# Kernel optimization log

Hardware: AMD Instinct MI355X
Metric: run time of the kernel (lower is better)

## Reference

```python
import jax, jax.numpy as jnp
import numpy as np

N_LAYERS = 2
DEPTH = 4
HIDDEN = 1024
INPUT = 1024
SEQ = 512
BATCH = 64


def setup_inputs() -> dict:
    key = jax.random.key(0)
    k1, k2, k3 = jax.random.split(key, 3)
    x = jax.random.normal(k1, (SEQ, BATCH, INPUT), dtype=jnp.float32)
    state = jnp.zeros((N_LAYERS, BATCH, HIDDEN), dtype=jnp.float32)
    # input_lin (no bias): layer 0 maps INPUT->2H, layers>0 map HIDDEN->2H (equal here)
    w_in = jax.random.normal(k2, (N_LAYERS, INPUT, 2 * HIDDEN), dtype=jnp.float32) * 0.03
    # hidden_lin per depth: HIDDEN->2H with bias
    w_h = jax.random.normal(k3, (N_LAYERS, DEPTH, HIDDEN, 2 * HIDDEN), dtype=jnp.float32) * 0.03
    b_h = jnp.zeros((N_LAYERS, DEPTH, 2 * HIDDEN), dtype=jnp.float32)
    return {"x": x, "state": state, "w_in": w_in, "w_h": w_h, "b_h": b_h}


def _cell(inp, s, w_in_l, w_h_l, b_h_l):
    # inp, s: [B, H]; one RHN cell = DEPTH highway micro-steps
    hg0 = inp @ w_in_l  # [B, 2H], only enters at depth 0
    for d in range(DEPTH):
        hg = s @ w_h_l[d] + b_h_l[d]
        if d == 0:
            hg = hg + hg0
        h = jnp.tanh(hg[:, :HIDDEN])
        g = jax.nn.sigmoid(hg[:, HIDDEN:])
        s = h * g + s * (1.0 - g)  # weight-tied carry: c = 1 - g
    return s


def reference(x, state, w_in, w_h, b_h):
    def step(s_all, x_t):
        inp = x_t
        new_s = []
        for l in range(N_LAYERS):
            s_l = _cell(inp, s_all[l], w_in[l], w_h[l], b_h[l])
            new_s.append(s_l)
            inp = s_l
        new_s = jnp.stack(new_s)  # [n_layers, B, H]
        return new_s, new_s[-1]

    final_s, out = jax.lax.scan(step, state, x)
    return out, final_s
```

## Files before the change

kernel.cpp:

```cpp
#include <hip/hip_runtime.h>
#include <math.h>
#include <stdint.h>


#define SEQ 512
#define NB 64
#define HID 1024
#define NH2 2048
#define NL 2
#define ND 4
#define SBUF (NB * HID)
#define WSLOT ((size_t)NH2 * (size_t)HID)
#define MROWS (SEQ * NB)

typedef _Float16 half8 __attribute__((ext_vector_type(8)));
typedef float float4v __attribute__((ext_vector_type(4)));

#define OFF_HG0 ((size_t)10 * WSLOT * 2)
#define OFF_SSEQ (OFF_HG0 + (size_t)MROWS * NH2 * 2)
#define OFF_MIR (OFF_SSEQ + (size_t)MROWS * HID * 2)
#define OFF_CAR (OFF_MIR + (size_t)4 * SBUF * 2)
#define OFF_CNT (OFF_CAR + (size_t)2 * SBUF * 4)

__device__ __forceinline__ half8 ld8(const _Float16* p) {
    return *reinterpret_cast<const half8*>(p);
}

__device__ __forceinline__ half8 cvt8(const float* p) {
    const float4v a = *reinterpret_cast<const float4v*>(p);
    const float4v b = *reinterpret_cast<const float4v*>(p + 4);
    half8 r;
    r[0] = (_Float16)a[0]; r[1] = (_Float16)a[1];
    r[2] = (_Float16)a[2]; r[3] = (_Float16)a[3];
    r[4] = (_Float16)b[0]; r[5] = (_Float16)b[1];
    r[6] = (_Float16)b[2]; r[7] = (_Float16)b[3];
    return r;
}

__global__ __launch_bounds__(256) void wprep(const float* __restrict__ w_in,
                                             const float* __restrict__ w_h,
                                             _Float16* __restrict__ Wt) {
    const int bid = (int)blockIdx.x;
    const int tk = bid & 31;
    const int tn = (bid >> 5) & 63;
    const int slot = bid >> 11;
    const int l = slot / 5;
    const int j = slot - l * 5;
    const float* __restrict__ src = (j == 0)
        ? (w_in + (size_t)l * WSLOT)
        : (w_h + (size_t)(l * ND + (j - 1)) * WSLOT);
    __shared__ float tile[32][33];
    const int tx = (int)(threadIdx.x & 31u);
    const int ty = (int)(threadIdx.x >> 5);
    const int n = tn * 32 + tx;
#pragma unroll
    for (int r = 0; r < 4; ++r) {
        const int k = tk * 32 + ty + r * 8;
        tile[ty + r * 8][tx] = src[(size_t)k * NH2 + n];
    }
    __syncthreads();
    _Float16* __restrict__ dst = Wt + (size_t)slot * WSLOT;
#pragma unroll
    for (int r = 0; r < 4; ++r) {
        const int nn = tn * 32 + ty + r * 8;
        const int kk = tk * 32 + tx;
        dst[(size_t)nn * HID + kk] = (_Float16)tile[tx][ty + r * 8];
    }
}

__global__ void sinit2(const float* __restrict__ state, _Float16* __restrict__ mir0,
                       float* __restrict__ car0, _Float16* __restrict__ mir1,
                       float* __restrict__ car1, int* __restrict__ cnts) {
    const int i = (int)(blockIdx.x * 256 + threadIdx.x);
    if (i < SBUF) {
        const float v0 = state[i];
        const float v1 = state[SBUF + i];
        mir0[i] = (_Float16)v0; car0[i] = v0;
        mir1[i] = (_Float16)v1; car1[i] = v1;
    }
    if (i < 256) cnts[i] = 0;
}

template <bool AF16>
__global__ __launch_bounds__(256) void gemm_proj(const void* __restrict__ Av,
                                                 const _Float16* __restrict__ Bslot,
                                                 _Float16* __restrict__ C) {
    const int bid = (int)blockIdx.x;
    const int nt = bid & 31;
    const int mt = bid >> 5;
    const int lane = (int)(threadIdx.x & 63u);
    const int wv = (int)(threadIdx.x >> 6);
    const int lr = lane & 15;
    const int kofs = (lane >> 4) * 8;
    const int m = mt * 64 + wv * 16 + lr;
    float4v acc[4];
#pragma unroll
    for (int i = 0; i < 4; ++i) acc[i] = (float4v){0.f, 0.f, 0.f, 0.f};
#pragma unroll 4
    for (int kb = 0; kb < 32; ++kb) {
        half8 a;
        if (AF16) a = ld8((const _Float16*)Av + (size_t)m * HID + kb * 32 + kofs);
        else      a = cvt8((const float*)Av + (size_t)m * HID + kb * 32 + kofs);
#pragma unroll
        for (int ct = 0; ct < 4; ++ct) {
            const int n = nt * 64 + ct * 16 + lr;
            half8 b = ld8(Bslot + (size_t)n * HID + kb * 32 + kofs);
            acc[ct] = __builtin_amdgcn_mfma_f32_16x16x32_f16(a, b, acc[ct], 0, 0, 0);
        }
    }
#pragma unroll
    for (int ct = 0; ct < 4; ++ct) {
#pragma unroll
        for (int i = 0; i < 4; ++i) {
            const int row = mt * 64 + wv * 16 + (lane >> 4) * 4 + i;
            const int col = nt * 64 + ct * 16 + lr;
            const unsigned short mine =
                __builtin_bit_cast(unsigned short, (_Float16)acc[ct][i]);
            const unsigned short oth = (unsigned short)__shfl_xor((int)mine, 1, 64);
            if ((lane & 1) == 0) {
                const uint32_t pk = (uint32_t)mine | ((uint32_t)oth << 16);
                *reinterpret_cast<uint32_t*>(C + (size_t)row * NH2 + col) = pk;
            }
        }
    }
}

__global__ __launch_bounds__(256) void rhn_scan(
    const _Float16* __restrict__ Wt, int slotBase,
    const float* __restrict__ bias,
    const _Float16* __restrict__ hg0,
    _Float16* __restrict__ mirA, _Float16* __restrict__ mirB,
    float* __restrict__ carry,
    int* __restrict__ cnt,
    _Float16* __restrict__ sseq,
    float* __restrict__ outp,
    float* __restrict__ fout) {
    extern __shared__ _Float16 lds[];
    const int wg = (int)blockIdx.x;
    const int d = wg >> 6;
    const int cg = wg & 63;
    const int tid = (int)threadIdx.x;
    const int lane = tid & 63;
    const int m0 = (tid >> 6) * 16;
    const int lr = lane & 15;
    const int kofs = (lane >> 4) * 8;
    const _Float16* __restrict__ slot = Wt + (size_t)(slotBase + d) * WSLOT;

    for (int i = 0; i < 16; ++i) {
        const int flat = i * 256 + tid;
        const int tile = flat >> 11;
        const int kb = (flat >> 6) & 31;
        const int ln = flat & 63;
        const int col = tile * HID + cg * 16 + (ln & 15);
        *reinterpret_cast<half8*>(lds + (size_t)flat * 8) =
            ld8(slot + (size_t)col * HID + kb * 32 + (ln >> 4) * 8);
    }
    __syncthreads();

    const int colh = cg * 16 + lr;
    const float bh = bias[d * NH2 + colh];
    const float bg = bias[d * NH2 + HID + colh];
    const int* __restrict__ pc = cnt + (((d + 3) & 3) * 32);
    int* __restrict__ myc = cnt + d * 32;

    for (int t = 0; t < SEQ; ++t) {
        const int gp = t * 4 + d;

        float pre_h[4], pre_g[4];
        if (d == 0) {
#pragma unroll
            for (int i = 0; i < 4; ++i) {
                const int gr = m0 + (lane >> 4) * 4 + i;
                const size_t hb = (size_t)(t * NB + gr) * NH2 + colh;
                pre_h[i] = (float)hg0[hb];
                pre_g[i] = (float)hg0[hb + HID];
            }
            __asm__ __volatile__("" :: "v"(pre_h[0]), "v"(pre_h[1]), "v"(pre_h[2]),
                                 "v"(pre_h[3]), "v"(pre_g[0]), "v"(pre_g[1]),
                                 "v"(pre_g[2]), "v"(pre_g[3]));
        }

        const int target = (d == 0) ? 64 * t : 64 * (t + 1);
        if (tid == 0) {
            while (__hip_atomic_load(pc, __ATOMIC_RELAXED, __HIP_MEMORY_SCOPE_AGENT) <
                   target) {
            }
        }
        __syncthreads();
        __builtin_amdgcn_fence(__ATOMIC_ACQUIRE, "agent");

        float sold[4];
#pragma unroll
        for (int i = 0; i < 4; ++i) {
            const int gr = m0 + (lane >> 4) * 4 + i;
            sold[i] = __hip_atomic_load(carry + (size_t)gr * HID + colh,
                                        __ATOMIC_RELAXED, __HIP_MEMORY_SCOPE_AGENT);
        }
        __asm__ __volatile__("" :: "v"(sold[0]), "v"(sold[1]), "v"(sold[2]),
                             "v"(sold[3]));

        const _Float16* __restrict__ mr = (gp & 1) ? mirB : mirA;
        const _Float16* __restrict__ arow = mr + (size_t)(m0 + lr) * HID + kofs;
        float4v acch = {0.f, 0.f, 0.f, 0.f};
        float4v accg = {0.f, 0.f, 0.f, 0.f};
#pragma unroll 8
        for (int kb = 0; kb < 32; ++kb) {
            half8 a = ld8(arow + kb * 32);
            half8 bhf = *reinterpret_cast<const half8*>(lds + (size_t)(kb * 64 + lane) * 8);
            half8 bgf =
                *reinterpret_cast<const half8*>(lds + (size_t)((32 + kb) * 64 + lane) * 8);
            acch = __builtin_amdgcn_mfma_f32_16x16x32_f16(a, bhf, acch, 0, 0, 0);
            accg = __builtin_amdgcn_mfma_f32_16x16x32_f16(a, bgf, accg, 0, 0, 0);
        }

        _Float16* __restrict__ mw = ((gp + 1) & 1) ? mirB : mirA;
#pragma unroll
        for (int i = 0; i < 4; ++i) {
            const int gr = m0 + (lane >> 4) * 4 + i;
            const size_t idx = (size_t)gr * HID + colh;
            float ah = acch[i] + bh;
            float ag = accg[i] + bg;
            if (d == 0) {
                ah += pre_h[i];
                ag += pre_g[i];
            }
            const float hv = 1.0f - __fdividef(2.0f, __expf(2.0f * ah) + 1.0f);
            const float gv = __fdividef(1.0f, 1.0f + __expf(-ag));
            const float sn = hv * gv + sold[i] * (1.f - gv);
            __hip_atomic_store(carry + idx, sn, __ATOMIC_RELAXED,
                               __HIP_MEMORY_SCOPE_AGENT);
            const unsigned short mine = __builtin_bit_cast(unsigned short, (_Float16)sn);
            const unsigned short oth = (unsigned short)__shfl_xor((int)mine, 1, 64);
            const uint32_t pk = (uint32_t)mine | ((uint32_t)oth << 16);
            if ((lane & 1) == 0) {
                __hip_atomic_store(reinterpret_cast<uint32_t*>(mw + idx), pk,
                                   __ATOMIC_RELAXED, __HIP_MEMORY_SCOPE_AGENT);
            }
            if (d == 3) {
                if (sseq) {
                    if ((lane & 1) == 0)
                        *reinterpret_cast<uint32_t*>(sseq + (size_t)t * SBUF + idx) = pk;
                } else {
                    outp[(size_t)t * SBUF + idx] = sn;
                }
                if (t == SEQ - 1) fout[idx] = sn;
            }
        }
        __syncthreads();
        if (tid == 0)
            __hip_atomic_fetch_add(myc, 1, __ATOMIC_RELAXED, __HIP_MEMORY_SCOPE_AGENT);
    }
}

extern "C" void kernel_launch(void* const* d_in, const int* in_sizes, int n_in,
                              void* d_out, int out_size, void* d_ws, size_t ws_size,
                              hipStream_t stream) {
    (void)in_sizes; (void)n_in; (void)out_size; (void)ws_size;
    const float* x     = (const float*)d_in[0];
    const float* state = (const float*)d_in[1];
    const float* w_in  = (const float*)d_in[2];
    const float* w_h   = (const float*)d_in[3];
    const float* b_h   = (const float*)d_in[4];
    float* out = (float*)d_out;
    char* ws = (char*)d_ws;
    _Float16* Wt   = (_Float16*)ws;
    _Float16* HG0  = (_Float16*)(ws + OFF_HG0);
    _Float16* Sseq = (_Float16*)(ws + OFF_SSEQ);
    _Float16* mir0a = (_Float16*)(ws + OFF_MIR);
    _Float16* mir0b = mir0a + SBUF;
    _Float16* mir1a = mir0b + SBUF;
    _Float16* mir1b = mir1a + SBUF;
    float* car0 = (float*)(ws + OFF_CAR);
    float* car1 = car0 + SBUF;
    int* cnts = (int*)(ws + OFF_CNT);

    (void)hipFuncSetAttribute((const void*)rhn_scan,
                              hipFuncAttributeMaxDynamicSharedMemorySize, 65536);

    wprep<<<10 * 64 * 32, 256, 0, stream>>>(w_in, w_h, Wt);
    sinit2<<<(SBUF + 255) / 256, 256, 0, stream>>>(state, mir0a, car0, mir1a, car1, cnts);
    gemm_proj<false><<<512 * 32, 256, 0, stream>>>((const void*)x, Wt + 0 * WSLOT, HG0);
    rhn_scan<<<256, 256, 65536, stream>>>(Wt, 1, b_h, HG0, mir0a, mir0b, car0, cnts,
                                          Sseq, (float*)nullptr,
                                          out + (size_t)SEQ * SBUF);
    gemm_proj<true><<<512 * 32, 256, 0, stream>>>((const void*)Sseq, Wt + 5 * WSLOT, HG0);
    rhn_scan<<<256, 256, 65536, stream>>>(Wt, 6, b_h + (size_t)ND * NH2, HG0, mir1a,
                                          mir1b, car1, cnts + 128, (_Float16*)nullptr,
                                          out, out + (size_t)SEQ * SBUF + SBUF);
}
```

Baseline: 45.93 ms.

## Fuse both RHN layers into one wavefront-pipelined persistent scan kernel

Replaces the two sequential per-layer scan kernels and the layer-1 input projection GEMM with a single persistent kernel. Each step b runs layer 0 at time b and layer 1 at time b-1, keeping both layers' depth weights in 128KB of LDS. The layer-1 input projection is computed inline from the fresh layer-0 output, with its weights read from global memory. The single atomic counter is replaced by per-workgroup flags that each wavefront polls with __all, removing a __syncthreads. This halves the number of serial recurrence steps, but each step does more work, needs more LDS, and adds global weight reads on depth 0.

```diff
diff --git a/kernel.cpp b/kernel.cpp
--- a/kernel.cpp
+++ b/kernel.cpp
@@ -125,16 +125,21 @@
     }
 }
 
-__global__ __launch_bounds__(256) void rhn_scan(
-    const _Float16* __restrict__ Wt, int slotBase,
+#define WFRAG(lyr, tile, kb)                                                     \
+    (*reinterpret_cast<const half8*>(                                            \
+        lds + ((size_t)((lyr)*4096 + (tile)*2048 + (kb)*64 + lane)) * 8))
+
+__global__ __launch_bounds__(256) void rhn_fused(
+    const _Float16* __restrict__ Wt,
     const float* __restrict__ bias,
     const _Float16* __restrict__ hg0,
-    _Float16* __restrict__ mirA, _Float16* __restrict__ mirB,
-    float* __restrict__ carry,
-    int* __restrict__ cnt,
     _Float16* __restrict__ sseq,
+    _Float16* __restrict__ m0a, _Float16* __restrict__ m0b,
+    _Float16* __restrict__ m1a, _Float16* __restrict__ m1b,
+    float* __restrict__ car0, float* __restrict__ car1,
+    int* __restrict__ flags,
     float* __restrict__ outp,
-    float* __restrict__ fout) {
+    float* __restrict__ fout0, float* __restrict__ fout1) {
     extern __shared__ _Float16 lds[];
     const int wg = (int)blockIdx.x;
     const int d = wg >> 6;
@@ -144,13 +149,17 @@
     const int m0 = (tid >> 6) * 16;
     const int lr = lane & 15;
     const int kofs = (lane >> 4) * 8;
-    const _Float16* __restrict__ slot = Wt + (size_t)(slotBase + d) * WSLOT;
-
-    for (int i = 0; i < 16; ++i) {
+    const bool isD0 = (d == 0);
+
+    for (int i = 0; i < 32; ++i) {
         const int flat = i * 256 + tid;
-        const int tile = flat >> 11;
-        const int kb = (flat >> 6) & 31;
-        const int ln = flat & 63;
+        const int lyr = flat >> 12;
+        const int rem = flat & 4095;
+        const int tile = rem >> 11;
+        const int kb = (rem >> 6) & 31;
+        const int ln = rem & 63;
+        const _Float16* __restrict__ slot =
+            Wt + (size_t)((lyr ? 6 : 1) + d) * WSLOT;
         const int col = tile * HID + cg * 16 + (ln & 15);
         *reinterpret_cast<half8*>(lds + (size_t)flat * 8) =
             ld8(slot + (size_t)col * HID + kb * 32 + (ln >> 4) * 8);
@@ -158,20 +167,28 @@
     __syncthreads();
 
     const int colh = cg * 16 + lr;
-    const float bh = bias[d * NH2 + colh];
-    const float bg = bias[d * NH2 + HID + colh];
-    const int* __restrict__ pc = cnt + (((d + 3) & 3) * 32);
-    int* __restrict__ myc = cnt + d * 32;
-
-    for (int t = 0; t < SEQ; ++t) {
-        const int gp = t * 4 + d;
+    const float bh0 = bias[d * NH2 + colh];
+    const float bg0 = bias[d * NH2 + HID + colh];
+    const float bh1 = bias[(ND + d) * NH2 + colh];
+    const float bg1 = bias[(ND + d) * NH2 + HID + colh];
+    const int prev = (d + 3) & 3;
+    int* __restrict__ pfl = flags + prev * 64 + lane;
+    int* __restrict__ myf = flags + d * 64 + cg;
+    const _Float16* __restrict__ winp =
+        Wt + (size_t)5 * WSLOT + (size_t)(cg * 16 + lr) * HID + kofs;
+    const size_t WGOFF = (size_t)HID * HID;
+
+    for (int b = 0; b <= SEQ; ++b) {
+        const bool doL0 = (b < SEQ);
+        const bool doL1 = (b > 0);
+        const int t1 = b - 1;
 
         float pre_h[4], pre_g[4];
-        if (d == 0) {
-#pragma unroll
-            for (int i = 0; i < 4; ++i) {
-                const int gr = m0 + (lane >> 4) * 4 + i;
-                const size_t hb = (size_t)(t * NB + gr) * NH2 + colh;
+        if (isD0 && doL0) {
+#pragma unroll
+            for (int i = 0; i < 4; ++i) {
+                const int gr = m0 + (lane >> 4) * 4 + i;
+                const size_t hb = (size_t)(b * NB + gr) * NH2 + colh;
                 pre_h[i] = (float)hg0[hb];
                 pre_g[i] = (float)hg0[hb + HID];
             }
@@ -180,75 +197,161 @@
                                  "v"(pre_g[2]), "v"(pre_g[3]));
         }
 
-        const int target = (d == 0) ? 64 * t : 64 * (t + 1);
-        if (tid == 0) {
-            while (__hip_atomic_load(pc, __ATOMIC_RELAXED, __HIP_MEMORY_SCOPE_AGENT) <
-                   target) {
-            }
-        }
-        __syncthreads();
+        const int target = isD0 ? b : b + 1;
+        if (target > 0) {
+            while (true) {
+                const int v =
+                    __hip_atomic_load(pfl, __ATOMIC_RELAXED, __HIP_MEMORY_SCOPE_AGENT);
+                if (__all(v >= target)) break;
+            }
+        }
         __builtin_amdgcn_fence(__ATOMIC_ACQUIRE, "agent");
 
-        float sold[4];
-#pragma unroll
-        for (int i = 0; i < 4; ++i) {
-            const int gr = m0 + (lane >> 4) * 4 + i;
-            sold[i] = __hip_atomic_load(carry + (size_t)gr * HID + colh,
-                                        __ATOMIC_RELAXED, __HIP_MEMORY_SCOPE_AGENT);
-        }
-        __asm__ __volatile__("" :: "v"(sold[0]), "v"(sold[1]), "v"(sold[2]),
-                             "v"(sold[3]));
-
-        const _Float16* __restrict__ mr = (gp & 1) ? mirB : mirA;
-        const _Float16* __restrict__ arow = mr + (size_t)(m0 + lr) * HID + kofs;
-        float4v acch = {0.f, 0.f, 0.f, 0.f};
-        float4v accg = {0.f, 0.f, 0.f, 0.f};
+        float sold0[4], sold1[4];
+        if (doL0) {
+#pragma unroll
+            for (int i = 0; i < 4; ++i) {
+                const int gr = m0 + (lane >> 4) * 4 + i;
+                sold0[i] = __hip_atomic_load(car0 + (size_t)gr * HID + colh,
+                                             __ATOMIC_RELAXED, __HIP_MEMORY_SCOPE_AGENT);
+            }
+            __asm__ __volatile__("" :: "v"(sold0[0]), "v"(sold0[1]), "v"(sold0[2]),
+                                 "v"(sold0[3]));
+        }
+        if (doL1) {
+#pragma unroll
+            for (int i = 0; i < 4; ++i) {
+                const int gr = m0 + (lane >> 4) * 4 + i;
+                sold1[i] = __hip_atomic_load(car1 + (size_t)gr * HID + colh,
+                                             __ATOMIC_RELAXED, __HIP_MEMORY_SCOPE_AGENT);
+            }
+            __asm__ __volatile__("" :: "v"(sold1[0]), "v"(sold1[1]), "v"(sold1[2]),
+                                 "v"(sold1[3]));
+        }
+
+        const int gp0 = b * 4 + d;
+        const int gp1 = t1 * 4 + d;
+        const _Float16* __restrict__ a0p =
+            ((gp0 & 1) ? m0b : m0a) + (size_t)(m0 + lr) * HID + kofs;
+        const _Float16* __restrict__ a1p =
+            ((gp1 & 1) ? m1b : m1a) + (size_t)(m0 + lr) * HID + kofs;
+        const _Float16* __restrict__ a2p =
+            sseq + ((size_t)t1 * NB + (m0 + lr)) * HID + kofs;
+
+        float4v acch0 = {0.f, 0.f, 0.f, 0.f}, accg0 = {0.f, 0.f, 0.f, 0.f};
+        float4v acch1 = {0.f, 0.f, 0.f, 0.f}, accg1 = {0.f, 0.f, 0.f, 0.f};
+
+        if (doL0 && doL1) {
+            if (isD0) {
+#pragma unroll 4
+                for (int kb = 0; kb < 32; ++kb) {
+                    half8 a0 = ld8(a0p + kb * 32);
+                    half8 a1 = ld8(a1p + kb * 32);
+                    half8 a2 = ld8(a2p + kb * 32);
+                    acch0 = __builtin_amdgcn_mfma_f32_16x16x32_f16(a0, WFRAG(0, 0, kb), acch0, 0, 0, 0);
+                    accg0 = __builtin_amdgcn_mfma_f32_16x16x32_f16(a0, WFRAG(0, 1, kb), accg0, 0, 0, 0);
+                    acch1 = __builtin_amdgcn_mfma_f32_16x16x32_f16(a1, WFRAG(1, 0, kb), acch1, 0, 0, 0);
+                    accg1 = __builtin_amdgcn_mfma_f32_16x16x32_f16(a1, WFRAG(1, 1, kb), accg1, 0, 0, 0);
+                    acch1 = __builtin_amdgcn_mfma_f32_16x16x32_f16(a2, ld8(winp + (size_t)kb * 32), acch1, 0, 0, 0);
+                    accg1 = __builtin_amdgcn_mfma_f32_16x16x32_f16(a2, ld8(winp + WGOFF + kb * 32), accg1, 0, 0, 0);
+                }
+            } else {
 #pragma unroll 8
-        for (int kb = 0; kb < 32; ++kb) {
-            half8 a = ld8(arow + kb * 32);
-            half8 bhf = *reinterpret_cast<const half8*>(lds + (size_t)(kb * 64 + lane) * 8);
-            half8 bgf =
-                *reinterpret_cast<const half8*>(lds + (size_t)((32 + kb) * 64 + lane) * 8);
-            acch = __builtin_amdgcn_mfma_f32_16x16x32_f16(a, bhf, acch, 0, 0, 0);
-            accg = __builtin_amdgcn_mfma_f32_16x16x32_f16(a, bgf, accg, 0, 0, 0);
-        }
-
-        _Float16* __restrict__ mw = ((gp + 1) & 1) ? mirB : mirA;
-#pragma unroll
-        for (int i = 0; i < 4; ++i) {
-            const int gr = m0 + (lane >> 4) * 4 + i;
-            const size_t idx = (size_t)gr * HID + colh;
-            float ah = acch[i] + bh;
-            float ag = accg[i] + bg;
-            if (d == 0) {
-                ah += pre_h[i];
-                ag += pre_g[i];
-            }
-            const float hv = 1.0f - __fdividef(2.0f, __expf(2.0f * ah) + 1.0f);
-            const float gv = __fdividef(1.0f, 1.0f + __expf(-ag));
-            const float sn = hv * gv + sold[i] * (1.f - gv);
-            __hip_atomic_store(carry + idx, sn, __ATOMIC_RELAXED,
-                               __HIP_MEMORY_SCOPE_AGENT);
-            const unsigned short mine = __builtin_bit_cast(unsigned short, (_Float16)sn);
-            const unsigned short oth = (unsigned short)__shfl_xor((int)mine, 1, 64);
-            const uint32_t pk = (uint32_t)mine | ((uint32_t)oth << 16);
-            if ((lane & 1) == 0) {
-                __hip_atomic_store(reinterpret_cast<uint32_t*>(mw + idx), pk,
-                                   __ATOMIC_RELAXED, __HIP_MEMORY_SCOPE_AGENT);
-            }
-            if (d == 3) {
-                if (sseq) {
-                    if ((lane & 1) == 0)
-                        *reinterpret_cast<uint32_t*>(sseq + (size_t)t * SBUF + idx) = pk;
-                } else {
-                    outp[(size_t)t * SBUF + idx] = sn;
-                }
-                if (t == SEQ - 1) fout[idx] = sn;
+                for (int kb = 0; kb < 32; ++kb) {
+                    half8 a0 = ld8(a0p + kb * 32);
+                    half8 a1 = ld8(a1p + kb * 32);
+                    acch0 = __builtin_amdgcn_mfma_f32_16x16x32_f16(a0, WFRAG(0, 0, kb), acch0, 0, 0, 0);
+                    accg0 = __builtin_amdgcn_mfma_f32_16x16x32_f16(a0, WFRAG(0, 1, kb), accg0, 0, 0, 0);
+                    acch1 = __builtin_amdgcn_mfma_f32_16x16x32_f16(a1, WFRAG(1, 0, kb), acch1, 0, 0, 0);
+                    accg1 = __builtin_amdgcn_mfma_f32_16x16x32_f16(a1, WFRAG(1, 1, kb), accg1, 0, 0, 0);
+                }
+            }
+        } else if (doL0) {
+#pragma unroll 8
+            for (int kb = 0; kb < 32; ++kb) {
+                half8 a0 = ld8(a0p + kb * 32);
+                acch0 = __builtin_amdgcn_mfma_f32_16x16x32_f16(a0, WFRAG(0, 0, kb), acch0, 0, 0, 0);
+                accg0 = __builtin_amdgcn_mfma_f32_16x16x32_f16(a0, WFRAG(0, 1, kb), accg0, 0, 0, 0);
+            }
+        } else {
+            if (isD0) {
+#pragma unroll 8
+                for (int kb = 0; kb < 32; ++kb) {
+                    half8 a1 = ld8(a1p + kb * 32);
+                    half8 a2 = ld8(a2p + kb * 32);
+                    acch1 = __builtin_amdgcn_mfma_f32_16x16x32_f16(a1, WFRAG(1, 0, kb), acch1, 0, 0, 0);
+                    accg1 = __builtin_amdgcn_mfma_f32_16x16x32_f16(a1, WFRAG(1, 1, kb), accg1, 0, 0, 0);
+                    acch1 = __builtin_amdgcn_mfma_f32_16x16x32_f16(a2, ld8(winp + (size_t)kb * 32), acch1, 0, 0, 0);
+                    accg1 = __builtin_amdgcn_mfma_f32_16x16x32_f16(a2, ld8(winp + WGOFF + kb * 32), accg1, 0, 0, 0);
+                }
+            } else {
+#pragma unroll 8
+                for (int kb = 0; kb < 32; ++kb) {
+                    half8 a1 = ld8(a1p + kb * 32);
+                    acch1 = __builtin_amdgcn_mfma_f32_16x16x32_f16(a1, WFRAG(1, 0, kb), acch1, 0, 0, 0);
+                    accg1 = __builtin_amdgcn_mfma_f32_16x16x32_f16(a1, WFRAG(1, 1, kb), accg1, 0, 0, 0);
+                }
+            }
+        }
+
+        if (doL0) {
+            _Float16* __restrict__ mw = ((gp0 + 1) & 1) ? m0b : m0a;
+#pragma unroll
+            for (int i = 0; i < 4; ++i) {
+                const int gr = m0 + (lane >> 4) * 4 + i;
+                const size_t idx = (size_t)gr * HID + colh;
+                float ah = acch0[i] + bh0;
+                float ag = accg0[i] + bg0;
+                if (isD0) { ah += pre_h[i]; ag += pre_g[i]; }
+                const float hv = 1.0f - __fdividef(2.0f, __expf(2.0f * ah) + 1.0f);
+                const float gv = __fdividef(1.0f, 1.0f + __expf(-ag));
+                const float sn = hv * gv + sold0[i] * (1.f - gv);
+                __hip_atomic_store(car0 + idx, sn, __ATOMIC_RELAXED,
+                                   __HIP_MEMORY_SCOPE_AGENT);
+                const unsigned short mine = __builtin_bit_cast(unsigned short, (_Float16)sn);
+                const unsigned short oth = (unsigned short)__shfl_xor((int)mine, 1, 64);
+                const uint32_t pk = (uint32_t)mine | ((uint32_t)oth << 16);
+                if ((lane & 1) == 0) {
+                    __hip_atomic_store(reinterpret_cast<uint32_t*>(mw + idx), pk,
+                                       __ATOMIC_RELAXED, __HIP_MEMORY_SCOPE_AGENT);
+                    if (d == 3) {
+                        __hip_atomic_store(
+                            reinterpret_cast<uint32_t*>(sseq + (size_t)b * SBUF + idx),
+                            pk, __ATOMIC_RELAXED, __HIP_MEMORY_SCOPE_AGENT);
+                    }
+                }
+                if (d == 3 && b == SEQ - 1) fout0[idx] = sn;
+            }
+        }
+        if (doL1) {
+            _Float16* __restrict__ mw = ((gp1 + 1) & 1) ? m1b : m1a;
+#pragma unroll
+            for (int i = 0; i < 4; ++i) {
+                const int gr = m0 + (lane >> 4) * 4 + i;
+                const size_t idx = (size_t)gr * HID + colh;
+                const float ah = acch1[i] + bh1;
+                const float ag = accg1[i] + bg1;
+                const float hv = 1.0f - __fdividef(2.0f, __expf(2.0f * ah) + 1.0f);
+                const float gv = __fdividef(1.0f, 1.0f + __expf(-ag));
+                const float sn = hv * gv + sold1[i] * (1.f - gv);
+                __hip_atomic_store(car1 + idx, sn, __ATOMIC_RELAXED,
+                                   __HIP_MEMORY_SCOPE_AGENT);
+                const unsigned short mine = __builtin_bit_cast(unsigned short, (_Float16)sn);
+                const unsigned short oth = (unsigned short)__shfl_xor((int)mine, 1, 64);
+                const uint32_t pk = (uint32_t)mine | ((uint32_t)oth << 16);
+                if ((lane & 1) == 0) {
+                    __hip_atomic_store(reinterpret_cast<uint32_t*>(mw + idx), pk,
+                                       __ATOMIC_RELAXED, __HIP_MEMORY_SCOPE_AGENT);
+                }
+                if (d == 3) {
+                    outp[(size_t)t1 * SBUF + idx] = sn;
+                    if (t1 == SEQ - 1) fout1[idx] = sn;
+                }
             }
         }
         __syncthreads();
         if (tid == 0)
-            __hip_atomic_fetch_add(myc, 1, __ATOMIC_RELAXED, __HIP_MEMORY_SCOPE_AGENT);
+            __hip_atomic_store(myf, b + 1, __ATOMIC_RELAXED, __HIP_MEMORY_SCOPE_AGENT);
     }
 }
 
@@ -272,19 +375,15 @@
     _Float16* mir1b = mir1a + SBUF;
     float* car0 = (float*)(ws + OFF_CAR);
     float* car1 = car0 + SBUF;
-    int* cnts = (int*)(ws + OFF_CNT);
-
-    (void)hipFuncSetAttribute((const void*)rhn_scan,
-                              hipFuncAttributeMaxDynamicSharedMemorySize, 65536);
+    int* flags = (int*)(ws + OFF_CNT);
+
+    (void)hipFuncSetAttribute((const void*)rhn_fused,
+                              hipFuncAttributeMaxDynamicSharedMemorySize, 131072);
 
     wprep<<<10 * 64 * 32, 256, 0, stream>>>(w_in, w_h, Wt);
-    sinit2<<<(SBUF + 255) / 256, 256, 0, stream>>>(state, mir0a, car0, mir1a, car1, cnts);
+    sinit2<<<(SBUF + 255) / 256, 256, 0, stream>>>(state, mir0a, car0, mir1a, car1, flags);
     gemm_proj<false><<<512 * 32, 256, 0, stream>>>((const void*)x, Wt + 0 * WSLOT, HG0);
-    rhn_scan<<<256, 256, 65536, stream>>>(Wt, 1, b_h, HG0, mir0a, mir0b, car0, cnts,
-                                          Sseq, (float*)nullptr,
-                                          out + (size_t)SEQ * SBUF);
-    gemm_proj<true><<<512 * 32, 256, 0, stream>>>((const void*)Sseq, Wt + 5 * WSLOT, HG0);
-    rhn_scan<<<256, 256, 65536, stream>>>(Wt, 6, b_h + (size_t)ND * NH2, HG0, mir1a,
-                                          mir1b, car1, cnts + 128, (_Float16*)nullptr,
-                                          out, out + (size_t)SEQ * SBUF + SBUF);
-}
+    rhn_fused<<<256, 256, 131072, stream>>>(
+        Wt, b_h, HG0, Sseq, mir0a, mir0b, mir1a, mir1b, car0, car1, flags,
+        out, out + (size_t)SEQ * SBUF, out + (size_t)SEQ * SBUF + SBUF);
+}
```

After: 38.64 ms. -15.9%, faster.
